# Optimization experiments

Hardware: AMD Instinct MI355X
Metric: run time of the kernel (lower is better)

## Reference

```python
import jax, jax.numpy as jnp
import numpy as np

TEMPERATURE = 0.1
LOSS_SCALE = 1.0
LAMBD = 0.5


def setup_inputs() -> dict:
    key = jax.random.key(0)
    k1, k2 = jax.random.split(key)
    B, D = 4096, 768
    predicted = jax.random.normal(k1, (B, D), dtype=jnp.float32)
    target = jax.random.normal(k2, (B, D), dtype=jnp.float32)
    return {"predicted": predicted, "target": target}


def reference(predicted, target):
    predicted = predicted.astype(jnp.float32)
    target = target.astype(jnp.float32)
    B = predicted.shape[0]

    # Pairwise L2 distances via Gram identity (avoids B x B x D intermediate):
    # ||p_i - t_j||^2 = ||p_i||^2 + ||t_j||^2 - 2 p_i . t_j
    p_sq = jnp.sum(predicted * predicted, axis=-1)  # [B]
    t_sq = jnp.sum(target * target, axis=-1)        # [B]
    cross = predicted @ target.T                    # [B, B]
    sq_dist = p_sq[:, None] + t_sq[None, :] - 2.0 * cross
    distances = jnp.sqrt(jnp.maximum(sq_dist, 0.0))  # [B, B]

    logits = -distances / TEMPERATURE
    # cross-entropy with labels = arange(B): mean of -log_softmax diagonal
    log_probs = jax.nn.log_softmax(logits, axis=-1)
    contrastive_dist_loss = -jnp.mean(jnp.diagonal(log_probs))

    # normalized L1 magnitude loss
    elementwise_l1 = jnp.sum(jnp.abs(predicted - target), axis=-1)  # [B]
    target_magnitude = jnp.sum(jnp.abs(target), axis=-1)            # [B]
    norm_factor = jax.lax.stop_gradient(target_magnitude)
    normalized_magnitude_loss = jnp.mean(elementwise_l1 / norm_factor)

    total_loss = LOSS_SCALE * (
        LAMBD * contrastive_dist_loss + (1.0 - LAMBD) * normalized_magnitude_loss
    )
    return (total_loss, contrastive_dist_loss, normalized_magnitude_loss)
```

## Files before the change

### kernel.cpp

```cpp
#include <hip/hip_runtime.h>
#include <hip/hip_bf16.h>
#include <math.h>

#define B_ROWS 4096
#define D_DIM  768

#define BM 128
#define BN 128
#define BK 32
#define NKT (D_DIM / 64)
#define KT_STRIDE (B_ROWS * 32)
#define HALF_USH 8192
#define NBLK ((B_ROWS / BM) * (B_ROWS / BN))

typedef __attribute__((ext_vector_type(8))) short bf16x8;
typedef __attribute__((ext_vector_type(4))) float f32x4;

__device__ __forceinline__ unsigned short f32_to_bf16(float x) {
    unsigned int u = __float_as_uint(x);
    return (unsigned short)((u + 0x7fffu + ((u >> 16) & 1u)) >> 16);
}

__device__ __forceinline__ void async_copy16(const unsigned short* g, unsigned short* l) {
    __builtin_amdgcn_global_load_lds(
        (const __attribute__((address_space(1))) unsigned int*)g,
        (__attribute__((address_space(3))) unsigned int*)l,
        16, 0, 0);
}

__global__ void __launch_bounds__(256) rowstats_kernel(
    const float* __restrict__ P, const float* __restrict__ T,
    unsigned short* __restrict__ Pb, unsigned short* __restrict__ Tb,
    float* __restrict__ p_sq, float* __restrict__ t_sq,
    float* __restrict__ diagl, float* __restrict__ magr,
    float* __restrict__ rowsum)
{
    const int wave = threadIdx.x >> 6, lane = threadIdx.x & 63;
    const int i = blockIdx.x * 4 + wave;
    const f32x4* prow = (const f32x4*)(P + (size_t)i * D_DIM);
    const f32x4* trow = (const f32x4*)(T + (size_t)i * D_DIM);
    const int swz = (i >> 1) & 3;

    float psq = 0.f, tsq = 0.f, cr = 0.f, l1 = 0.f, tm = 0.f;
    #pragma unroll
    for (int u = 0; u < 3; ++u) {
        const int c4 = u * 64 + lane;
        f32x4 p = prow[c4], t = trow[c4];
        #pragma unroll
        for (int k = 0; k < 4; ++k) {
            psq += p[k] * p[k]; tsq += t[k] * t[k]; cr += p[k] * t[k];
            l1 += fabsf(p[k] - t[k]); tm += fabsf(t[k]);
        }
        const int kt  = c4 >> 3;
        const int cc  = (c4 >> 1) & 3;
        const int sub = c4 & 1;
        const size_t doff = (size_t)kt * KT_STRIDE + (size_t)i * 32
                          + (size_t)(((cc ^ swz) << 3) + (sub << 2));
        *(ushort4*)(Pb + doff) = make_ushort4(f32_to_bf16(p[0]), f32_to_bf16(p[1]),
                                              f32_to_bf16(p[2]), f32_to_bf16(p[3]));
        *(ushort4*)(Tb + doff) = make_ushort4(f32_to_bf16(t[0]), f32_to_bf16(t[1]),
                                              f32_to_bf16(t[2]), f32_to_bf16(t[3]));
    }
    #pragma unroll
    for (int m = 1; m < 64; m <<= 1) {
        psq += __shfl_xor(psq, m, 64);
        tsq += __shfl_xor(tsq, m, 64);
        cr  += __shfl_xor(cr,  m, 64);
        l1  += __shfl_xor(l1,  m, 64);
        tm  += __shfl_xor(tm,  m, 64);
    }
    if (lane == 0) {
        p_sq[i] = psq;
        t_sq[i] = tsq;
        float sq = fmaxf(psq + tsq - 2.0f * cr, 0.0f);
        diagl[i] = -sqrtf(sq) * 10.0f;
        magr[i]  = l1 / tm;
        rowsum[i] = 0.0f;
    }
}

__global__ void __launch_bounds__(256) lse_gemm_kernel(
    const unsigned short* __restrict__ Pb, const unsigned short* __restrict__ Tb,
    const float* __restrict__ p_sq, const float* __restrict__ t_sq,
    const float* __restrict__ diagl, float* __restrict__ rowsum)
{
    __shared__ __align__(16) unsigned short S[2 * HALF_USH];

    const int tid  = threadIdx.x;
    const int lane = tid & 63, wave = tid >> 6;

    const int flat = blockIdx.x;
    const int xcd  = flat & 7;
    const int s    = flat >> 3;
    const int ti   = ((xcd & 1) << 4) + (s & 15);
    const int tj   = ((xcd >> 1) << 3) + (s >> 4);
    const int i0   = ti * BM, j0 = tj * BN;

    const int wm = wave >> 1, wn = wave & 1;
    const int row16 = lane & 15, quad = lane >> 4;
    const int slot  = quad ^ ((row16 >> 1) & 3);

    int aoff[4], boff[4];
    #pragma unroll
    for (int mt = 0; mt < 4; ++mt)
        aoff[mt] = (wm * 64 + mt * 16 + row16) * BK + (slot << 3);
    #pragma unroll
    for (int nt = 0; nt < 4; ++nt)
        boff[nt] = 4096 + (wn * 64 + nt * 16 + row16) * BK + (slot << 3);

    const int  sub  = wave >> 1;
    const bool isB  = wave & 1;
    const unsigned short* gsrc = isB ? Tb : Pb;
    const int  r0g  = isB ? j0 : i0;
    const unsigned short* gp[8];
    int lb[8];
    #pragma unroll
    for (int k = 0; k < 8; ++k) {
        gp[k] = gsrc + (size_t)sub * KT_STRIDE
                     + (size_t)(r0g + k * 16) * 32 + lane * 8;
        lb[k] = sub * HALF_USH + (isB ? 4096 : 0) + k * 512;
    }

    f32x4 acc[4][4];
    #pragma unroll
    for (int a = 0; a < 4; ++a)
        #pragma unroll
        for (int b = 0; b < 4; ++b)
            acc[a][b] = (f32x4){0.f, 0.f, 0.f, 0.f};

    for (int kt = 0; kt < NKT; ++kt) {
        const size_t koff = (size_t)(2 * kt) * KT_STRIDE;
        #pragma unroll
        for (int k = 0; k < 8; ++k)
            async_copy16(gp[k] + koff, &S[lb[k]]);
        __syncthreads();

        #pragma unroll
        for (int h = 0; h < 2; ++h) {
            const unsigned short* base = &S[h * HALF_USH];
            bf16x8 a[4], b[4];
            #pragma unroll
            for (int mt = 0; mt < 4; ++mt) a[mt] = *(const bf16x8*)(base + aoff[mt]);
            #pragma unroll
            for (int nt = 0; nt < 4; ++nt) b[nt] = *(const bf16x8*)(base + boff[nt]);
            __builtin_amdgcn_s_setprio(1);
            #pragma unroll
            for (int mt = 0; mt < 4; ++mt)
                #pragma unroll
                for (int nt = 0; nt < 4; ++nt)
                    acc[mt][nt] = __builtin_amdgcn_mfma_f32_16x16x32_bf16(
                        a[mt], b[nt], acc[mt][nt], 0, 0, 0);
            __builtin_amdgcn_s_setprio(0);
        }
        __syncthreads();
    }

    const float NT_LOG2E = -14.4269504089f;
    const float LOG2E    = 1.44269504089f;
    float tsq_l[4];
    #pragma unroll
    for (int nt = 0; nt < 4; ++nt)
        tsq_l[nt] = t_sq[j0 + wn * 64 + nt * 16 + row16];

    #pragma unroll
    for (int mt = 0; mt < 4; ++mt) {
        #pragma unroll
        for (int r = 0; r < 4; ++r) {
            const int i = i0 + wm * 64 + mt * 16 + quad * 4 + r;
            const float psq = p_sq[i];
            const float c0  = -diagl[i] * LOG2E;
            float sfin = 0.f;
            #pragma unroll
            for (int nt = 0; nt < 4; ++nt) {
                float c  = acc[mt][nt][r];
                float sq = fmaxf(fmaf(-2.0f, c, psq + tsq_l[nt]), 0.0f);
                float d  = sqrtf(sq);
                float y  = fmaf(d, NT_LOG2E, c0);
                sfin += exp2f(y);
            }
            #pragma unroll
            for (int m = 1; m < 16; m <<= 1) sfin += __shfl_xor(sfin, m, 64);
            if (row16 == 0) atomicAdd(&rowsum[i], sfin);
        }
    }
}

__global__ void __launch_bounds__(256) finalize_kernel(
    const float* __restrict__ rowsum, const float* __restrict__ magr,
    float* __restrict__ out)
{
    const int tid = threadIdx.x;
    double sc = 0.0, sm = 0.0;
    for (int i = tid; i < B_ROWS; i += 256) {
        sc += log((double)rowsum[i]);
        sm += (double)magr[i];
    }
    #pragma unroll
    for (int m = 1; m < 64; m <<= 1) {
        sc += __shfl_xor(sc, m, 64);
        sm += __shfl_xor(sm, m, 64);
    }
    __shared__ double red[4][2];
    const int wave = tid >> 6, lane = tid & 63;
    if (lane == 0) { red[wave][0] = sc; red[wave][1] = sm; }
    __syncthreads();
    if (tid == 0) {
        sc = red[0][0] + red[1][0] + red[2][0] + red[3][0];
        sm = red[0][1] + red[1][1] + red[2][1] + red[3][1];
        double lc = sc / (double)B_ROWS;
        double lm = sm / (double)B_ROWS;
        out[0] = (float)(0.5 * lc + 0.5 * lm);
        out[1] = (float)lc;
        out[2] = (float)lm;
    }
}

extern "C" void kernel_launch(void* const* d_in, const int* in_sizes, int n_in,
                              void* d_out, int out_size, void* d_ws, size_t ws_size,
                              hipStream_t stream) {
    const float* P = (const float*)d_in[0];
    const float* T = (const float*)d_in[1];
    float* out = (float*)d_out;

    char* ws = (char*)d_ws;
    float* rowsum = (float*)ws;               ws += B_ROWS * sizeof(float);
    float* p_sq   = (float*)ws;               ws += B_ROWS * sizeof(float);
    float* t_sq   = (float*)ws;               ws += B_ROWS * sizeof(float);
    float* diagl  = (float*)ws;               ws += B_ROWS * sizeof(float);
    float* magr   = (float*)ws;               ws += B_ROWS * sizeof(float);
    unsigned short* Pb = (unsigned short*)ws; ws += (size_t)B_ROWS * D_DIM * 2;
    unsigned short* Tb = (unsigned short*)ws;

    rowstats_kernel<<<B_ROWS / 4, 256, 0, stream>>>(
        P, T, Pb, Tb, p_sq, t_sq, diagl, magr, rowsum);
    lse_gemm_kernel<<<NBLK, 256, 0, stream>>>(
        Pb, Tb, p_sq, t_sq, diagl, rowsum);
    finalize_kernel<<<1, 256, 0, stream>>>(rowsum, magr, out);
}
```

Before: 131.9 us.

## Load GEMM operands directly from global into registers with double buffering

Drops the LDS staging and barriers from the fused distance/logsumexp GEMM. Each wave now loads its A and B bf16 fragments straight from the pre-swizzled global layout into registers, prefetching the next K-slice while MFMAs run on the current one. Launch bounds request 3 blocks per CU. Removing shared memory cuts the barrier stalls, but each fragment is now fetched by two waves instead of one, which relies on L2/L1 caching and raises register pressure.

```diff
diff --git a/kernel.cpp b/kernel.cpp
--- a/kernel.cpp
+++ b/kernel.cpp
@@ -8,9 +8,8 @@
 #define BM 128
 #define BN 128
 #define BK 32
-#define NKT (D_DIM / 64)
+#define NKT (D_DIM / BK)
 #define KT_STRIDE (B_ROWS * 32)
-#define HALF_USH 8192
 #define NBLK ((B_ROWS / BM) * (B_ROWS / BN))
 
 typedef __attribute__((ext_vector_type(8))) short bf16x8;
@@ -19,13 +18,6 @@
 __device__ __forceinline__ unsigned short f32_to_bf16(float x) {
     unsigned int u = __float_as_uint(x);
     return (unsigned short)((u + 0x7fffu + ((u >> 16) & 1u)) >> 16);
-}
-
-__device__ __forceinline__ void async_copy16(const unsigned short* g, unsigned short* l) {
-    __builtin_amdgcn_global_load_lds(
-        (const __attribute__((address_space(1))) unsigned int*)g,
-        (__attribute__((address_space(3))) unsigned int*)l,
-        16, 0, 0);
 }
 
 __global__ void __launch_bounds__(256) rowstats_kernel(
@@ -79,13 +71,11 @@
     }
 }
 
-__global__ void __launch_bounds__(256) lse_gemm_kernel(
+__global__ void __launch_bounds__(256, 3) lse_gemm_kernel(
     const unsigned short* __restrict__ Pb, const unsigned short* __restrict__ Tb,
     const float* __restrict__ p_sq, const float* __restrict__ t_sq,
     const float* __restrict__ diagl, float* __restrict__ rowsum)
 {
-    __shared__ __align__(16) unsigned short S[2 * HALF_USH];
-
     const int tid  = threadIdx.x;
     const int lane = tid & 63, wave = tid >> 6;
 
@@ -100,26 +90,14 @@
     const int row16 = lane & 15, quad = lane >> 4;
     const int slot  = quad ^ ((row16 >> 1) & 3);
 
-    int aoff[4], boff[4];
+    const unsigned short* ap[4];
+    const unsigned short* bp[4];
     #pragma unroll
     for (int mt = 0; mt < 4; ++mt)
-        aoff[mt] = (wm * 64 + mt * 16 + row16) * BK + (slot << 3);
+        ap[mt] = Pb + (size_t)(i0 + wm * 64 + mt * 16 + row16) * 32 + slot * 8;
     #pragma unroll
     for (int nt = 0; nt < 4; ++nt)
-        boff[nt] = 4096 + (wn * 64 + nt * 16 + row16) * BK + (slot << 3);
-
-    const int  sub  = wave >> 1;
-    const bool isB  = wave & 1;
-    const unsigned short* gsrc = isB ? Tb : Pb;
-    const int  r0g  = isB ? j0 : i0;
-    const unsigned short* gp[8];
-    int lb[8];
-    #pragma unroll
-    for (int k = 0; k < 8; ++k) {
-        gp[k] = gsrc + (size_t)sub * KT_STRIDE
-                     + (size_t)(r0g + k * 16) * 32 + lane * 8;
-        lb[k] = sub * HALF_USH + (isB ? 4096 : 0) + k * 512;
-    }
+        bp[nt] = Tb + (size_t)(j0 + wn * 64 + nt * 16 + row16) * 32 + slot * 8;
 
     f32x4 acc[4][4];
     #pragma unroll
@@ -128,31 +106,49 @@
         for (int b = 0; b < 4; ++b)
             acc[a][b] = (f32x4){0.f, 0.f, 0.f, 0.f};
 
-    for (int kt = 0; kt < NKT; ++kt) {
-        const size_t koff = (size_t)(2 * kt) * KT_STRIDE;
-        #pragma unroll
-        for (int k = 0; k < 8; ++k)
-            async_copy16(gp[k] + koff, &S[lb[k]]);
-        __syncthreads();
-
-        #pragma unroll
-        for (int h = 0; h < 2; ++h) {
-            const unsigned short* base = &S[h * HALF_USH];
-            bf16x8 a[4], b[4];
-            #pragma unroll
-            for (int mt = 0; mt < 4; ++mt) a[mt] = *(const bf16x8*)(base + aoff[mt]);
-            #pragma unroll
-            for (int nt = 0; nt < 4; ++nt) b[nt] = *(const bf16x8*)(base + boff[nt]);
-            __builtin_amdgcn_s_setprio(1);
-            #pragma unroll
-            for (int mt = 0; mt < 4; ++mt)
-                #pragma unroll
-                for (int nt = 0; nt < 4; ++nt)
-                    acc[mt][nt] = __builtin_amdgcn_mfma_f32_16x16x32_bf16(
-                        a[mt], b[nt], acc[mt][nt], 0, 0, 0);
-            __builtin_amdgcn_s_setprio(0);
-        }
-        __syncthreads();
+    bf16x8 a0[4], b0[4], a1[4], b1[4];
+
+    #pragma unroll
+    for (int f = 0; f < 4; ++f) {
+        a0[f] = *(const bf16x8*)(ap[f]);
+        b0[f] = *(const bf16x8*)(bp[f]);
+    }
+
+    #pragma unroll
+    for (int t = 0; t < NKT; t += 2) {
+        {
+            const size_t o1 = (size_t)(t + 1) * KT_STRIDE;
+            #pragma unroll
+            for (int f = 0; f < 4; ++f) {
+                a1[f] = *(const bf16x8*)(ap[f] + o1);
+                b1[f] = *(const bf16x8*)(bp[f] + o1);
+            }
+        }
+        __builtin_amdgcn_s_setprio(1);
+        #pragma unroll
+        for (int mt = 0; mt < 4; ++mt)
+            #pragma unroll
+            for (int nt = 0; nt < 4; ++nt)
+                acc[mt][nt] = __builtin_amdgcn_mfma_f32_16x16x32_bf16(
+                    a0[mt], b0[nt], acc[mt][nt], 0, 0, 0);
+        __builtin_amdgcn_s_setprio(0);
+
+        if (t + 2 < NKT) {
+            const size_t o2 = (size_t)(t + 2) * KT_STRIDE;
+            #pragma unroll
+            for (int f = 0; f < 4; ++f) {
+                a0[f] = *(const bf16x8*)(ap[f] + o2);
+                b0[f] = *(const bf16x8*)(bp[f] + o2);
+            }
+        }
+        __builtin_amdgcn_s_setprio(1);
+        #pragma unroll
+        for (int mt = 0; mt < 4; ++mt)
+            #pragma unroll
+            for (int nt = 0; nt < 4; ++nt)
+                acc[mt][nt] = __builtin_amdgcn_mfma_f32_16x16x32_bf16(
+                    a1[mt], b1[nt], acc[mt][nt], 0, 0, 0);
+        __builtin_amdgcn_s_setprio(0);
     }
 
     const float NT_LOG2E = -14.4269504089f;
```

Result: faster. 121.2 us (-8.1%).
